# Kernel tuning notes

Measured on AMD Instinct MI355X. Metric: run time of the kernel, lower is better.

The kernel has to match this reference:

```python
import jax, jax.numpy as jnp
import numpy as np

N_NODES = 50000
N_EDGES = 640000
D = 128      # in_feats
OUT = 128    # out_feats


def setup_inputs() -> dict:
    key = jax.random.key(0)
    ks = jax.random.split(key, 8)
    feat = jax.random.normal(ks[0], (N_NODES, D), dtype=jnp.float32)
    weight = jax.random.uniform(ks[1], (N_EDGES,), dtype=jnp.float32)
    src = jax.random.randint(ks[2], (N_EDGES,), 0, N_NODES, dtype=jnp.int64)
    dst = jax.random.randint(ks[3], (N_EDGES,), 0, N_NODES, dtype=jnp.int64)
    # xavier_uniform with relu gain ~ sqrt(2)*sqrt(6/(fan_in+fan_out))
    g = np.sqrt(2.0)
    lim_pool = g * np.sqrt(6.0 / (D + D))
    lim_neigh = g * np.sqrt(6.0 / (2 * D + OUT))
    W_pool = jax.random.uniform(ks[4], (D, D), dtype=jnp.float32, minval=-lim_pool, maxval=lim_pool)
    b_pool = jnp.zeros((D,), dtype=jnp.float32)
    W_neigh = jax.random.uniform(ks[5], (OUT, 2 * D), dtype=jnp.float32, minval=-lim_neigh, maxval=lim_neigh)
    b_neigh = jnp.zeros((OUT,), dtype=jnp.float32)
    return {"feat": feat, "weight": weight, "src": src, "dst": dst,
            "W_pool": W_pool, "b_pool": b_pool, "W_neigh": W_neigh, "b_neigh": b_neigh}


def reference(feat, weight, src, dst, W_pool, b_pool, W_neigh, b_neigh):
    n = feat.shape[0]
    # fc_pool: h = feat @ W_pool.T + b_pool  -> [N, D]
    h = feat @ W_pool.T + b_pool
    # u_mul_e: per-edge message m_e = h[src_e] * w_e  -> [E, D]
    m = h[src] * weight[:, None]
    # max reduce over incoming edges (scatter-max by dst)
    neigh = jax.ops.segment_max(m, dst, num_segments=n)
    # zero-degree nodes get 0 (segment_max fills empties with -inf)
    deg = jax.ops.segment_sum(jnp.ones_like(weight), dst, num_segments=n)
    neigh = jnp.where(deg[:, None] > 0, neigh, jnp.zeros((), dtype=feat.dtype))
    # fc_neigh on concat(feat, neigh)
    rst = jnp.concatenate([feat, neigh], axis=1) @ W_neigh.T + b_neigh
    return rst
```

## Files before the change

### kernel.cpp

```cpp
#include <hip/hip_runtime.h>
#include <cstdint>
#include <cstddef>

#define N_NODES 50000
#define N_EDGES 640000
#define DF 128

#define NBUCK 196
#define BCAP  6144
#define ECAP  8192
#define PA_BLOCKS 250
#define DUMMY_ROW 50000

typedef __attribute__((ext_vector_type(8))) short bf16x8;
typedef __attribute__((ext_vector_type(4))) float f32x4;

__device__ inline unsigned short f2bf(float f) {
    unsigned int u = __float_as_uint(f);
    return (unsigned short)((u + 0x7fffu + ((u >> 16) & 1u)) >> 16);
}

#define NF4 (N_NODES * DF / 4)
#define NWG (3 * 2048)
__global__ __launch_bounds__(256) void k1_setup_bucket(
    const float* __restrict__ feat,
    const float* __restrict__ W_pool,
    const float* __restrict__ W_neigh,
    const int* __restrict__ src,
    const int* __restrict__ dst,
    const float* __restrict__ w,
    unsigned short* __restrict__ featb,
    unsigned short* __restrict__ hb,
    unsigned short* __restrict__ Wp_f,
    unsigned short* __restrict__ Wn1_f,
    unsigned short* __restrict__ Wn2_f,
    int* __restrict__ bucketcnt,
    uint2* __restrict__ staging)
{
    int bid = blockIdx.x;
    int t = threadIdx.x;
    if (bid < PA_BLOCKS) {
        __shared__ int cnt[NBUCK];
        __shared__ int runbase[NBUCK];
        int base = bid * 2560;
        if (t < NBUCK) cnt[t] = 0;
        __syncthreads();
        uint2 rec[10];
        int bk[10];
        #pragma unroll
        for (int i = 0; i < 10; ++i) {
            int e = base + i * 256 + t;
            int s = src[e], d = dst[e];
            bk[i] = d >> 8;
            rec[i].x = (unsigned int)s | ((unsigned int)(d & 255) << 16);
            rec[i].y = __float_as_uint(w[e]);
            atomicAdd(&cnt[bk[i]], 1);
        }
        __syncthreads();
        if (t < NBUCK) {
            runbase[t] = atomicAdd(&bucketcnt[t], cnt[t]);
            cnt[t] = 0;
        }
        __syncthreads();
        #pragma unroll
        for (int i = 0; i < 10; ++i) {
            int r = atomicAdd(&cnt[bk[i]], 1);
            int pos = runbase[bk[i]] + r;
            if (pos < BCAP) staging[bk[i] * BCAP + pos] = rec[i];
        }
    } else if (bid < 250 + NF4 / 256) {
        int idx = (bid - PA_BLOCKS) * 256 + t;
        float4 v = ((const float4*)feat)[idx];
        ushort4 o;
        o.x = f2bf(v.x); o.y = f2bf(v.y); o.z = f2bf(v.z); o.w = f2bf(v.w);
        ((ushort4*)featb)[idx] = o;
    } else if (bid < 250 + NF4 / 256 + NWG / 256) {
        int g = (bid - PA_BLOCKS - NF4 / 256) * 256 + t;
        int m = g >> 11;
        int r8 = g & 2047;
        int L = r8 & 63, tt = (r8 >> 6) & 3, c = r8 >> 8;
        int o = c * 16 + (L & 15);
        int kb = tt * 32 + (L >> 4) * 8;
        const float* srcp;
        unsigned short* dstp;
        if (m == 0)      { srcp = W_pool  + o * 128 + kb;       dstp = Wp_f;  }
        else if (m == 1) { srcp = W_neigh + o * 256 + kb;       dstp = Wn1_f; }
        else             { srcp = W_neigh + o * 256 + 128 + kb; dstp = Wn2_f; }
        ushort4 lo, hi;
        float4 a = ((const float4*)srcp)[0];
        float4 b = ((const float4*)srcp)[1];
        lo.x = f2bf(a.x); lo.y = f2bf(a.y); lo.z = f2bf(a.z); lo.w = f2bf(a.w);
        hi.x = f2bf(b.x); hi.y = f2bf(b.y); hi.z = f2bf(b.z); hi.w = f2bf(b.w);
        ((ushort4*)(dstp + r8 * 8))[0] = lo;
        ((ushort4*)(dstp + r8 * 8))[1] = hi;
    } else {
        if (t < DF) hb[(size_t)DUMMY_ROW * DF + t] = 0xFF7Fu;
    }
}

#define GEMMB 196
__global__ __launch_bounds__(1024) void k2_gemm_passb(
    const unsigned short* __restrict__ featb,
    const unsigned short* __restrict__ Wp_f,
    const float* __restrict__ b_pool,
    unsigned short* __restrict__ hb,
    const int* __restrict__ bucketcnt,
    const uint2* __restrict__ staging,
    int* __restrict__ offsets,
    int* __restrict__ nend,
    uint2* __restrict__ edges)
{
    int t = threadIdx.x;
    if (blockIdx.x < GEMMB) {
        int wave = blockIdx.x * 16 + (t >> 6);
        int lane = t & 63;
        int m0 = wave * 16;
        if (m0 >= N_NODES) return;
        const int n = lane & 15, quad = lane >> 4;

        f32x4 acc[8];
        #pragma unroll
        for (int c = 0; c < 8; ++c) {
            float bv = b_pool[c * 16 + n];
            acc[c] = (f32x4){bv, bv, bv, bv};
        }
        const unsigned short* aptr = featb + (size_t)(m0 + n) * DF + quad * 8;
        #pragma unroll
        for (int tt = 0; tt < 4; ++tt) {
            bf16x8 af = *(const bf16x8*)(aptr + tt * 32);
            #pragma unroll
            for (int c = 0; c < 8; ++c) {
                bf16x8 bf = *(const bf16x8*)(Wp_f + (size_t)((c * 4 + tt) * 64 + lane) * 8);
                acc[c] = __builtin_amdgcn_mfma_f32_16x16x32_bf16(af, bf, acc[c], 0, 0, 0);
            }
        }
        #pragma unroll
        for (int c = 0; c < 8; ++c)
            #pragma unroll
            for (int r = 0; r < 4; ++r)
                hb[(size_t)(m0 + quad * 4 + r) * DF + c * 16 + n] = f2bf(acc[c][r]);
    } else {
        __shared__ int dcnt[256];
        __shared__ int sc[256];
        int b = blockIdx.x - GEMMB;
        int cnt = bucketcnt[b];
        if (cnt > BCAP) cnt = BCAP;

        if (t < 256) dcnt[t] = 0;
        __syncthreads();

        uint2 rec[6];
        int nit = (cnt + 1023) >> 10;
        for (int i = 0; i < nit; ++i) {
            int idx = i * 1024 + t;
            if (idx < cnt) {
                rec[i] = staging[(size_t)b * BCAP + idx];
                atomicAdd(&dcnt[(rec[i].x >> 16) & 255], 1);
            }
        }
        __syncthreads();
        int mydeg = 0, mypad = 0;
        if (t < 256) {
            mydeg = dcnt[t];
            mypad = (mydeg + 7) & ~7;
            sc[t] = mypad;
        }
        __syncthreads();
        #pragma unroll
        for (int off = 1; off < 256; off <<= 1) {
            int u = (t < 256 && t >= off) ? sc[t - off] : 0;
            __syncthreads();
            if (t < 256) sc[t] += u;
            __syncthreads();
        }
        if (t < 256) {
            int beg = b * ECAP + sc[t] - mypad;
            int node = b * 256 + t;
            if (node < N_NODES) {
                offsets[node] = beg;
                nend[node] = beg + mypad;
            }
            dcnt[t] = beg;
            uint2 dmy; dmy.x = DUMMY_ROW; dmy.y = 0x3F800000u;
            for (int k = mydeg; k < mypad; ++k) edges[beg + k] = dmy;
        }
        __syncthreads();
        for (int i = 0; i < nit; ++i) {
            int idx = i * 1024 + t;
            if (idx < cnt) {
                int dl = (rec[i].x >> 16) & 255;
                int pos = atomicAdd(&dcnt[dl], 1);
                uint2 fin;
                fin.x = rec[i].x & 0xFFFFu;
                fin.y = rec[i].y;
                edges[pos] = fin;
            }
        }
    }
}

__global__ __launch_bounds__(256) void neigh_max_kernel(
    const unsigned short* __restrict__ hb, const int* __restrict__ offsets,
    const int* __restrict__ nend,
    const uint2* __restrict__ edges,
    unsigned short* __restrict__ neighb)
{
    int gwave = (blockIdx.x * 256 + threadIdx.x) >> 6;
    if (gwave >= N_NODES) return;
    int node = __builtin_amdgcn_readfirstlane(gwave);
    int lane = threadIdx.x & 63;
    const int half = lane >> 5;
    const int q = lane & 31;

    int beg = offsets[node], end = nend[node];
    float4 acc = make_float4(-3.4e38f, -3.4e38f, -3.4e38f, -3.4e38f);

    for (int e = beg; e < end; e += 8) {
        uint2 e0 = edges[e],     e1 = edges[e + 1], e2 = edges[e + 2], e3 = edges[e + 3];
        uint2 e4 = edges[e + 4], e5 = edges[e + 5], e6 = edges[e + 6], e7 = edges[e + 7];
        uint2 mA = half ? e1 : e0;
        uint2 mB = half ? e3 : e2;
        uint2 mC = half ? e5 : e4;
        uint2 mD = half ? e7 : e6;
        float wA = __uint_as_float(mA.y);
        float wB = __uint_as_float(mB.y);
        float wC = __uint_as_float(mC.y);
        float wD = __uint_as_float(mD.y);
        uint2 pA = *(const uint2*)(hb + (size_t)mA.x * DF + q * 4);
        uint2 pB = *(const uint2*)(hb + (size_t)mB.x * DF + q * 4);
        uint2 pC = *(const uint2*)(hb + (size_t)mC.x * DF + q * 4);
        uint2 pD = *(const uint2*)(hb + (size_t)mD.x * DF + q * 4);
        acc.x = fmaxf(acc.x, __uint_as_float(pA.x << 16)          * wA);
        acc.y = fmaxf(acc.y, __uint_as_float(pA.x & 0xffff0000u)  * wA);
        acc.z = fmaxf(acc.z, __uint_as_float(pA.y << 16)          * wA);
        acc.w = fmaxf(acc.w, __uint_as_float(pA.y & 0xffff0000u)  * wA);
        acc.x = fmaxf(acc.x, __uint_as_float(pB.x << 16)          * wB);
        acc.y = fmaxf(acc.y, __uint_as_float(pB.x & 0xffff0000u)  * wB);
        acc.z = fmaxf(acc.z, __uint_as_float(pB.y << 16)          * wB);
        acc.w = fmaxf(acc.w, __uint_as_float(pB.y & 0xffff0000u)  * wB);
        acc.x = fmaxf(acc.x, __uint_as_float(pC.x << 16)          * wC);
        acc.y = fmaxf(acc.y, __uint_as_float(pC.x & 0xffff0000u)  * wC);
        acc.z = fmaxf(acc.z, __uint_as_float(pC.y << 16)          * wC);
        acc.w = fmaxf(acc.w, __uint_as_float(pC.y & 0xffff0000u)  * wC);
        acc.x = fmaxf(acc.x, __uint_as_float(pD.x << 16)          * wD);
        acc.y = fmaxf(acc.y, __uint_as_float(pD.x & 0xffff0000u)  * wD);
        acc.z = fmaxf(acc.z, __uint_as_float(pD.y << 16)          * wD);
        acc.w = fmaxf(acc.w, __uint_as_float(pD.y & 0xffff0000u)  * wD);
    }

    float4 o;
    o.x = fmaxf(acc.x, __shfl_xor(acc.x, 32));
    o.y = fmaxf(acc.y, __shfl_xor(acc.y, 32));
    o.z = fmaxf(acc.z, __shfl_xor(acc.z, 32));
    o.w = fmaxf(acc.w, __shfl_xor(acc.w, 32));
    if (beg == end) o = make_float4(0.f, 0.f, 0.f, 0.f);
    if (half == 0) {
        ushort4 ob;
        ob.x = f2bf(o.x); ob.y = f2bf(o.y); ob.z = f2bf(o.z); ob.w = f2bf(o.w);
        *(ushort4*)(neighb + (size_t)node * DF + q * 4) = ob;
    }
}

__global__ __launch_bounds__(256) void gemm_out(
    const unsigned short* __restrict__ featb,
    const unsigned short* __restrict__ neighb,
    const unsigned short* __restrict__ Wn1_f,
    const unsigned short* __restrict__ Wn2_f,
    const float* __restrict__ bias,
    float* __restrict__ out)
{
    int wave = (blockIdx.x * 256 + threadIdx.x) >> 6;
    int lane = threadIdx.x & 63;
    int m0 = wave * 16;
    if (m0 >= N_NODES) return;
    const int n = lane & 15, quad = lane >> 4;

    f32x4 acc[8];
    #pragma unroll
    for (int c = 0; c < 8; ++c) {
        float bv = bias[c * 16 + n];
        acc[c] = (f32x4){bv, bv, bv, bv};
    }

    const unsigned short* a0 = featb  + (size_t)(m0 + n) * DF + quad * 8;
    const unsigned short* a1 = neighb + (size_t)(m0 + n) * DF + quad * 8;
    #pragma unroll
    for (int t = 0; t < 4; ++t) {
        bf16x8 af = *(const bf16x8*)(a0 + t * 32);
        #pragma unroll
        for (int c = 0; c < 8; ++c) {
            bf16x8 bf = *(const bf16x8*)(Wn1_f + (size_t)((c * 4 + t) * 64 + lane) * 8);
            acc[c] = __builtin_amdgcn_mfma_f32_16x16x32_bf16(af, bf, acc[c], 0, 0, 0);
        }
    }
    #pragma unroll
    for (int t = 0; t < 4; ++t) {
        bf16x8 af = *(const bf16x8*)(a1 + t * 32);
        #pragma unroll
        for (int c = 0; c < 8; ++c) {
            bf16x8 bf = *(const bf16x8*)(Wn2_f + (size_t)((c * 4 + t) * 64 + lane) * 8);
            acc[c] = __builtin_amdgcn_mfma_f32_16x16x32_bf16(af, bf, acc[c], 0, 0, 0);
        }
    }

    #pragma unroll
    for (int c = 0; c < 8; ++c)
        #pragma unroll
        for (int r = 0; r < 4; ++r)
            out[(size_t)(m0 + quad * 4 + r) * DF + c * 16 + n] = acc[c][r];
}

extern "C" void kernel_launch(void* const* d_in, const int* in_sizes, int n_in,
                              void* d_out, int out_size, void* d_ws, size_t ws_size,
                              hipStream_t stream) {
    const float* feat    = (const float*)d_in[0];
    const float* weight  = (const float*)d_in[1];
    const int*   src     = (const int*)d_in[2];
    const int*   dst     = (const int*)d_in[3];
    const float* W_pool  = (const float*)d_in[4];
    const float* b_pool  = (const float*)d_in[5];
    const float* W_neigh = (const float*)d_in[6];
    const float* b_neigh = (const float*)d_in[7];
    float* out = (float*)d_out;

    char* ws = (char*)d_ws;
    unsigned short* featb  = (unsigned short*)(ws);
    unsigned short* hb     = (unsigned short*)(ws + 12800000);
    unsigned short* Wp_f   = (unsigned short*)(ws + 25600512);
    unsigned short* Wn1_f  = (unsigned short*)(ws + 25633280);
    unsigned short* Wn2_f  = (unsigned short*)(ws + 25666048);
    int*   offsets   = (int*)  (ws + 25698816);
    int*   nend      = (int*)  (ws + 25898816);
    int*   bucketcnt = (int*)  (ws + 26098816);
    uint2* staging   = (uint2*)(ws + 26099840);
    uint2* edges     = (uint2*)(ws + 35733632);
    unsigned short* neighb = (unsigned short*)(ws + 48578688);

    hipMemsetAsync(bucketcnt, 0, 1024, stream);

    const int K1_BLOCKS = PA_BLOCKS + NF4 / 256 + NWG / 256 + 1;
    k1_setup_bucket<<<K1_BLOCKS, 256, 0, stream>>>(
        feat, W_pool, W_neigh, src, dst, weight,
        featb, hb, Wp_f, Wn1_f, Wn2_f, bucketcnt, staging);

    k2_gemm_passb<<<GEMMB + NBUCK, 1024, 0, stream>>>(
        featb, Wp_f, b_pool, hb, bucketcnt, staging, offsets, nend, edges);

    neigh_max_kernel<<<(N_NODES + 3) / 4, 256, 0, stream>>>(
        hb, offsets, nend, edges, neighb);

    gemm_out<<<782, 256, 0, stream>>>(
        featb, neighb, Wn1_f, Wn2_f, b_neigh, out);
}
```

Before: 162.3 us.

## Replace two-pass bucket sort with fixed-slot atomic scatter and fuse pool GEMM

```diff
diff --git a/kernel.cpp b/kernel.cpp
--- a/kernel.cpp
+++ b/kernel.cpp
@@ -5,12 +5,11 @@
 #define N_NODES 50000
 #define N_EDGES 640000
 #define DF 128
-
-#define NBUCK 196
-#define BCAP  6144
-#define ECAP  8192
-#define PA_BLOCKS 250
-#define DUMMY_ROW 50000
+#define SLOT 64
+
+#define SC_BLOCKS 625
+#define GEMM_BLOCKS 782
+#define FRAG_BLOCKS 16
 
 typedef __attribute__((ext_vector_type(8))) short bf16x8;
 typedef __attribute__((ext_vector_type(4))) float f32x4;
@@ -20,72 +19,98 @@
     return (unsigned short)((u + 0x7fffu + ((u >> 16) & 1u)) >> 16);
 }
 
-#define NF4 (N_NODES * DF / 4)
-#define NWG (3 * 2048)
-__global__ __launch_bounds__(256) void k1_setup_bucket(
+__global__ __launch_bounds__(256) void k1_scatter_gemm(
     const float* __restrict__ feat,
     const float* __restrict__ W_pool,
     const float* __restrict__ W_neigh,
+    const float* __restrict__ b_pool,
     const int* __restrict__ src,
     const int* __restrict__ dst,
     const float* __restrict__ w,
     unsigned short* __restrict__ featb,
     unsigned short* __restrict__ hb,
-    unsigned short* __restrict__ Wp_f,
     unsigned short* __restrict__ Wn1_f,
     unsigned short* __restrict__ Wn2_f,
-    int* __restrict__ bucketcnt,
-    uint2* __restrict__ staging)
+    int* __restrict__ cnt,
+    uint2* __restrict__ edges)
 {
     int bid = blockIdx.x;
     int t = threadIdx.x;
-    if (bid < PA_BLOCKS) {
-        __shared__ int cnt[NBUCK];
-        __shared__ int runbase[NBUCK];
-        int base = bid * 2560;
-        if (t < NBUCK) cnt[t] = 0;
+    if (bid < SC_BLOCKS) {
+        int base = bid * 1024;
+        #pragma unroll
+        for (int k = 0; k < 4; ++k) {
+            int e = base + k * 256 + t;
+            int s = src[e], d = dst[e];
+            float wv = w[e];
+            int c = atomicAdd(&cnt[d], 1);
+            if (c < SLOT) {
+                uint2 r; r.x = (unsigned int)s; r.y = __float_as_uint(wv);
+                edges[(size_t)d * SLOT + c] = r;
+            }
+        }
+    } else if (bid < SC_BLOCKS + GEMM_BLOCKS) {
+        __shared__ __align__(16) unsigned short wsh[16384];
+        #pragma unroll
+        for (int k = 0; k < 8; ++k) {
+            int r8 = t * 8 + k;
+            int L = r8 & 63, tt2 = (r8 >> 6) & 3, c = r8 >> 8;
+            const float* srcp = W_pool + (c * 16 + (L & 15)) * 128
+                                       + tt2 * 32 + (L >> 4) * 8;
+            float4 a = ((const float4*)srcp)[0];
+            float4 b = ((const float4*)srcp)[1];
+            ushort4 lo, hi;
+            lo.x = f2bf(a.x); lo.y = f2bf(a.y); lo.z = f2bf(a.z); lo.w = f2bf(a.w);
+            hi.x = f2bf(b.x); hi.y = f2bf(b.y); hi.z = f2bf(b.z); hi.w = f2bf(b.w);
+            ((ushort4*)(wsh + r8 * 8))[0] = lo;
+            ((ushort4*)(wsh + r8 * 8))[1] = hi;
+        }
         __syncthreads();
-        uint2 rec[10];
-        int bk[10];
-        #pragma unroll
-        for (int i = 0; i < 10; ++i) {
-            int e = base + i * 256 + t;
-            int s = src[e], d = dst[e];
-            bk[i] = d >> 8;
-            rec[i].x = (unsigned int)s | ((unsigned int)(d & 255) << 16);
-            rec[i].y = __float_as_uint(w[e]);
-            atomicAdd(&cnt[bk[i]], 1);
-        }
-        __syncthreads();
-        if (t < NBUCK) {
-            runbase[t] = atomicAdd(&bucketcnt[t], cnt[t]);
-            cnt[t] = 0;
-        }
-        __syncthreads();
-        #pragma unroll
-        for (int i = 0; i < 10; ++i) {
-            int r = atomicAdd(&cnt[bk[i]], 1);
-            int pos = runbase[bk[i]] + r;
-            if (pos < BCAP) staging[bk[i] * BCAP + pos] = rec[i];
-        }
-    } else if (bid < 250 + NF4 / 256) {
-        int idx = (bid - PA_BLOCKS) * 256 + t;
-        float4 v = ((const float4*)feat)[idx];
-        ushort4 o;
-        o.x = f2bf(v.x); o.y = f2bf(v.y); o.z = f2bf(v.z); o.w = f2bf(v.w);
-        ((ushort4*)featb)[idx] = o;
-    } else if (bid < 250 + NF4 / 256 + NWG / 256) {
-        int g = (bid - PA_BLOCKS - NF4 / 256) * 256 + t;
+
+        int gwave = (bid - SC_BLOCKS) * 4 + (t >> 6);
+        int m0 = gwave * 16;
+        if (m0 < N_NODES) {
+            int lane = t & 63;
+            const int n = lane & 15, quad = lane >> 4;
+            f32x4 acc[8];
+            #pragma unroll
+            for (int c = 0; c < 8; ++c) {
+                float bv = b_pool[c * 16 + n];
+                acc[c] = (f32x4){bv, bv, bv, bv};
+            }
+            const float* fp = feat + (size_t)(m0 + n) * DF + quad * 8;
+            unsigned short* fbp = featb + (size_t)(m0 + n) * DF + quad * 8;
+            #pragma unroll
+            for (int tt = 0; tt < 4; ++tt) {
+                float4 a = ((const float4*)(fp + tt * 32))[0];
+                float4 b = ((const float4*)(fp + tt * 32))[1];
+                union { bf16x8 v; ushort4 u4[2]; } af;
+                af.u4[0].x = f2bf(a.x); af.u4[0].y = f2bf(a.y);
+                af.u4[0].z = f2bf(a.z); af.u4[0].w = f2bf(a.w);
+                af.u4[1].x = f2bf(b.x); af.u4[1].y = f2bf(b.y);
+                af.u4[1].z = f2bf(b.z); af.u4[1].w = f2bf(b.w);
+                *(bf16x8*)(fbp + tt * 32) = af.v;
+                #pragma unroll
+                for (int c = 0; c < 8; ++c) {
+                    bf16x8 bfv = *(const bf16x8*)(wsh + (size_t)((c * 4 + tt) * 64 + lane) * 8);
+                    acc[c] = __builtin_amdgcn_mfma_f32_16x16x32_bf16(af.v, bfv, acc[c], 0, 0, 0);
+                }
+            }
+            #pragma unroll
+            for (int c = 0; c < 8; ++c)
+                #pragma unroll
+                for (int r = 0; r < 4; ++r)
+                    hb[(size_t)(m0 + quad * 4 + r) * DF + c * 16 + n] = f2bf(acc[c][r]);
+        }
+    } else {
+        int g = (bid - SC_BLOCKS - GEMM_BLOCKS) * 256 + t;
         int m = g >> 11;
         int r8 = g & 2047;
         int L = r8 & 63, tt = (r8 >> 6) & 3, c = r8 >> 8;
         int o = c * 16 + (L & 15);
         int kb = tt * 32 + (L >> 4) * 8;
-        const float* srcp;
-        unsigned short* dstp;
-        if (m == 0)      { srcp = W_pool  + o * 128 + kb;       dstp = Wp_f;  }
-        else if (m == 1) { srcp = W_neigh + o * 256 + kb;       dstp = Wn1_f; }
-        else             { srcp = W_neigh + o * 256 + 128 + kb; dstp = Wn2_f; }
+        const float* srcp = W_neigh + o * 256 + (m ? 128 : 0) + kb;
+        unsigned short* dstp = m ? Wn2_f : Wn1_f;
         ushort4 lo, hi;
         float4 a = ((const float4*)srcp)[0];
         float4 b = ((const float4*)srcp)[1];
@@ -93,115 +118,12 @@
         hi.x = f2bf(b.x); hi.y = f2bf(b.y); hi.z = f2bf(b.z); hi.w = f2bf(b.w);
         ((ushort4*)(dstp + r8 * 8))[0] = lo;
         ((ushort4*)(dstp + r8 * 8))[1] = hi;
-    } else {
-        if (t < DF) hb[(size_t)DUMMY_ROW * DF + t] = 0xFF7Fu;
-    }
-}
-
-#define GEMMB 196
-__global__ __launch_bounds__(1024) void k2_gemm_passb(
-    const unsigned short* __restrict__ featb,
-    const unsigned short* __restrict__ Wp_f,
-    const float* __restrict__ b_pool,
-    unsigned short* __restrict__ hb,
-    const int* __restrict__ bucketcnt,
-    const uint2* __restrict__ staging,
-    int* __restrict__ offsets,
-    int* __restrict__ nend,
-    uint2* __restrict__ edges)
-{
-    int t = threadIdx.x;
-    if (blockIdx.x < GEMMB) {
-        int wave = blockIdx.x * 16 + (t >> 6);
-        int lane = t & 63;
-        int m0 = wave * 16;
-        if (m0 >= N_NODES) return;
-        const int n = lane & 15, quad = lane >> 4;
-
-        f32x4 acc[8];
-        #pragma unroll
-        for (int c = 0; c < 8; ++c) {
-            float bv = b_pool[c * 16 + n];
-            acc[c] = (f32x4){bv, bv, bv, bv};
-        }
-        const unsigned short* aptr = featb + (size_t)(m0 + n) * DF + quad * 8;
-        #pragma unroll
-        for (int tt = 0; tt < 4; ++tt) {
-            bf16x8 af = *(const bf16x8*)(aptr + tt * 32);
-            #pragma unroll
-            for (int c = 0; c < 8; ++c) {
-                bf16x8 bf = *(const bf16x8*)(Wp_f + (size_t)((c * 4 + tt) * 64 + lane) * 8);
-                acc[c] = __builtin_amdgcn_mfma_f32_16x16x32_bf16(af, bf, acc[c], 0, 0, 0);
-            }
-        }
-        #pragma unroll
-        for (int c = 0; c < 8; ++c)
-            #pragma unroll
-            for (int r = 0; r < 4; ++r)
-                hb[(size_t)(m0 + quad * 4 + r) * DF + c * 16 + n] = f2bf(acc[c][r]);
-    } else {
-        __shared__ int dcnt[256];
-        __shared__ int sc[256];
-        int b = blockIdx.x - GEMMB;
-        int cnt = bucketcnt[b];
-        if (cnt > BCAP) cnt = BCAP;
-
-        if (t < 256) dcnt[t] = 0;
-        __syncthreads();
-
-        uint2 rec[6];
-        int nit = (cnt + 1023) >> 10;
-        for (int i = 0; i < nit; ++i) {
-            int idx = i * 1024 + t;
-            if (idx < cnt) {
-                rec[i] = staging[(size_t)b * BCAP + idx];
-                atomicAdd(&dcnt[(rec[i].x >> 16) & 255], 1);
-            }
-        }
-        __syncthreads();
-        int mydeg = 0, mypad = 0;
-        if (t < 256) {
-            mydeg = dcnt[t];
-            mypad = (mydeg + 7) & ~7;
-            sc[t] = mypad;
-        }
-        __syncthreads();
-        #pragma unroll
-        for (int off = 1; off < 256; off <<= 1) {
-            int u = (t < 256 && t >= off) ? sc[t - off] : 0;
-            __syncthreads();
-            if (t < 256) sc[t] += u;
-            __syncthreads();
-        }
-        if (t < 256) {
-            int beg = b * ECAP + sc[t] - mypad;
-            int node = b * 256 + t;
-            if (node < N_NODES) {
-                offsets[node] = beg;
-                nend[node] = beg + mypad;
-            }
-            dcnt[t] = beg;
-            uint2 dmy; dmy.x = DUMMY_ROW; dmy.y = 0x3F800000u;
-            for (int k = mydeg; k < mypad; ++k) edges[beg + k] = dmy;
-        }
-        __syncthreads();
-        for (int i = 0; i < nit; ++i) {
-            int idx = i * 1024 + t;
-            if (idx < cnt) {
-                int dl = (rec[i].x >> 16) & 255;
-                int pos = atomicAdd(&dcnt[dl], 1);
-                uint2 fin;
-                fin.x = rec[i].x & 0xFFFFu;
-                fin.y = rec[i].y;
-                edges[pos] = fin;
-            }
-        }
     }
 }
 
 __global__ __launch_bounds__(256) void neigh_max_kernel(
-    const unsigned short* __restrict__ hb, const int* __restrict__ offsets,
-    const int* __restrict__ nend,
+    const unsigned short* __restrict__ hb,
+    const int* __restrict__ cnt,
     const uint2* __restrict__ edges,
     unsigned short* __restrict__ neighb)
 {
@@ -212,12 +134,21 @@
     const int half = lane >> 5;
     const int q = lane & 31;
 
-    int beg = offsets[node], end = nend[node];
+    int beg = node * SLOT;
+    int dg = cnt[node]; if (dg > SLOT) dg = SLOT;
+    int end = beg + dg;
     float4 acc = make_float4(-3.4e38f, -3.4e38f, -3.4e38f, -3.4e38f);
 
     for (int e = beg; e < end; e += 8) {
-        uint2 e0 = edges[e],     e1 = edges[e + 1], e2 = edges[e + 2], e3 = edges[e + 3];
-        uint2 e4 = edges[e + 4], e5 = edges[e + 5], e6 = edges[e + 6], e7 = edges[e + 7];
+        int i1 = min(e + 1, end - 1);
+        int i2 = min(e + 2, end - 1);
+        int i3 = min(e + 3, end - 1);
+        int i4 = min(e + 4, end - 1);
+        int i5 = min(e + 5, end - 1);
+        int i6 = min(e + 6, end - 1);
+        int i7 = min(e + 7, end - 1);
+        uint2 e0 = edges[e],  e1 = edges[i1], e2 = edges[i2], e3 = edges[i3];
+        uint2 e4 = edges[i4], e5 = edges[i5], e6 = edges[i6], e7 = edges[i7];
         uint2 mA = half ? e1 : e0;
         uint2 mB = half ? e3 : e2;
         uint2 mC = half ? e5 : e4;
@@ -253,7 +184,7 @@
     o.y = fmaxf(acc.y, __shfl_xor(acc.y, 32));
     o.z = fmaxf(acc.z, __shfl_xor(acc.z, 32));
     o.w = fmaxf(acc.w, __shfl_xor(acc.w, 32));
-    if (beg == end) o = make_float4(0.f, 0.f, 0.f, 0.f);
+    if (dg == 0) o = make_float4(0.f, 0.f, 0.f, 0.f);
     if (half == 0) {
         ushort4 ob;
         ob.x = f2bf(o.x); ob.y = f2bf(o.y); ob.z = f2bf(o.z); ob.w = f2bf(o.w);
@@ -326,28 +257,21 @@
     char* ws = (char*)d_ws;
     unsigned short* featb  = (unsigned short*)(ws);
     unsigned short* hb     = (unsigned short*)(ws + 12800000);
-    unsigned short* Wp_f   = (unsigned short*)(ws + 25600512);
-    unsigned short* Wn1_f  = (unsigned short*)(ws + 25633280);
-    unsigned short* Wn2_f  = (unsigned short*)(ws + 25666048);
-    int*   offsets   = (int*)  (ws + 25698816);
-    int*   nend      = (int*)  (ws + 25898816);
-    int*   bucketcnt = (int*)  (ws + 26098816);
-    uint2* staging   = (uint2*)(ws + 26099840);
-    uint2* edges     = (uint2*)(ws + 35733632);
-    unsigned short* neighb = (unsigned short*)(ws + 48578688);
-
-    hipMemsetAsync(bucketcnt, 0, 1024, stream);
-
-    const int K1_BLOCKS = PA_BLOCKS + NF4 / 256 + NWG / 256 + 1;
-    k1_setup_bucket<<<K1_BLOCKS, 256, 0, stream>>>(
-        feat, W_pool, W_neigh, src, dst, weight,
-        featb, hb, Wp_f, Wn1_f, Wn2_f, bucketcnt, staging);
-
-    k2_gemm_passb<<<GEMMB + NBUCK, 1024, 0, stream>>>(
-        featb, Wp_f, b_pool, hb, bucketcnt, staging, offsets, nend, edges);
+    unsigned short* Wn1_f  = (unsigned short*)(ws + 25600000);
+    unsigned short* Wn2_f  = (unsigned short*)(ws + 25632768);
+    int*   cnt       = (int*)  (ws + 25665536);
+    uint2* edges     = (uint2*)(ws + 25865536);
+    unsigned short* neighb = (unsigned short*)(ws + 51465536);
+
+    hipMemsetAsync(cnt, 0, N_NODES * sizeof(int), stream);
+
+    const int K1_BLOCKS = SC_BLOCKS + GEMM_BLOCKS + FRAG_BLOCKS;
+    k1_scatter_gemm<<<K1_BLOCKS, 256, 0, stream>>>(
+        feat, W_pool, W_neigh, b_pool, src, dst, weight,
+        featb, hb, Wn1_f, Wn2_f, cnt, edges);
 
     neigh_max_kernel<<<(N_NODES + 3) / 4, 256, 0, stream>>>(
-        hb, offsets, nend, edges, neighb);
+        hb, cnt, edges, neighb);
 
     gemm_out<<<782, 256, 0, stream>>>(
         featb, neighb, Wn1_f, Wn2_f, b_neigh, out);
```

Measured after the change: 171.1 us. 1.05x slower.

## Fuse feat bf16 conversion into GEMMs and stage W_pool fragments in LDS

Applied to the files above, without the earlier changes.

```diff
diff --git a/kernel.cpp b/kernel.cpp
--- a/kernel.cpp
+++ b/kernel.cpp
@@ -10,6 +10,7 @@
 #define BCAP  6144
 #define ECAP  8192
 #define PA_BLOCKS 250
+#define FRAG_BLOCKS 16
 #define DUMMY_ROW 50000
 
 typedef __attribute__((ext_vector_type(8))) short bf16x8;
@@ -20,18 +21,12 @@
     return (unsigned short)((u + 0x7fffu + ((u >> 16) & 1u)) >> 16);
 }
 
-#define NF4 (N_NODES * DF / 4)
-#define NWG (3 * 2048)
-__global__ __launch_bounds__(256) void k1_setup_bucket(
-    const float* __restrict__ feat,
-    const float* __restrict__ W_pool,
+__global__ __launch_bounds__(256) void k1_passa_frags(
     const float* __restrict__ W_neigh,
     const int* __restrict__ src,
     const int* __restrict__ dst,
     const float* __restrict__ w,
-    unsigned short* __restrict__ featb,
     unsigned short* __restrict__ hb,
-    unsigned short* __restrict__ Wp_f,
     unsigned short* __restrict__ Wn1_f,
     unsigned short* __restrict__ Wn2_f,
     int* __restrict__ bucketcnt,
@@ -68,24 +63,15 @@
             int pos = runbase[bk[i]] + r;
             if (pos < BCAP) staging[bk[i] * BCAP + pos] = rec[i];
         }
-    } else if (bid < 250 + NF4 / 256) {
-        int idx = (bid - PA_BLOCKS) * 256 + t;
-        float4 v = ((const float4*)feat)[idx];
-        ushort4 o;
-        o.x = f2bf(v.x); o.y = f2bf(v.y); o.z = f2bf(v.z); o.w = f2bf(v.w);
-        ((ushort4*)featb)[idx] = o;
-    } else if (bid < 250 + NF4 / 256 + NWG / 256) {
-        int g = (bid - PA_BLOCKS - NF4 / 256) * 256 + t;
+    } else if (bid < PA_BLOCKS + FRAG_BLOCKS) {
+        int g = (bid - PA_BLOCKS) * 256 + t;
         int m = g >> 11;
         int r8 = g & 2047;
         int L = r8 & 63, tt = (r8 >> 6) & 3, c = r8 >> 8;
         int o = c * 16 + (L & 15);
         int kb = tt * 32 + (L >> 4) * 8;
-        const float* srcp;
-        unsigned short* dstp;
-        if (m == 0)      { srcp = W_pool  + o * 128 + kb;       dstp = Wp_f;  }
-        else if (m == 1) { srcp = W_neigh + o * 256 + kb;       dstp = Wn1_f; }
-        else             { srcp = W_neigh + o * 256 + 128 + kb; dstp = Wn2_f; }
+        const float* srcp = W_neigh + o * 256 + (m ? 128 : 0) + kb;
+        unsigned short* dstp = m ? Wn2_f : Wn1_f;
         ushort4 lo, hi;
         float4 a = ((const float4*)srcp)[0];
         float4 b = ((const float4*)srcp)[1];
@@ -100,8 +86,8 @@
 
 #define GEMMB 196
 __global__ __launch_bounds__(1024) void k2_gemm_passb(
-    const unsigned short* __restrict__ featb,
-    const unsigned short* __restrict__ Wp_f,
+    const float* __restrict__ feat,
+    const float* __restrict__ W_pool,
     const float* __restrict__ b_pool,
     unsigned short* __restrict__ hb,
     const int* __restrict__ bucketcnt,
@@ -112,26 +98,48 @@
 {
     int t = threadIdx.x;
     if (blockIdx.x < GEMMB) {
+        __shared__ __align__(16) unsigned short wsh[16384];
+        #pragma unroll
+        for (int k = 0; k < 2; ++k) {
+            int r8 = k * 1024 + t;
+            int L = r8 & 63, tt2 = (r8 >> 6) & 3, c = r8 >> 8;
+            const float* srcp = W_pool + (c * 16 + (L & 15)) * 128
+                                       + tt2 * 32 + (L >> 4) * 8;
+            float4 a = ((const float4*)srcp)[0];
+            float4 b = ((const float4*)srcp)[1];
+            ushort4 lo, hi;
+            lo.x = f2bf(a.x); lo.y = f2bf(a.y); lo.z = f2bf(a.z); lo.w = f2bf(a.w);
+            hi.x = f2bf(b.x); hi.y = f2bf(b.y); hi.z = f2bf(b.z); hi.w = f2bf(b.w);
+            ((ushort4*)(wsh + r8 * 8))[0] = lo;
+            ((ushort4*)(wsh + r8 * 8))[1] = hi;
+        }
+        __syncthreads();
+
         int wave = blockIdx.x * 16 + (t >> 6);
-        int lane = t & 63;
         int m0 = wave * 16;
         if (m0 >= N_NODES) return;
+        int lane = t & 63;
         const int n = lane & 15, quad = lane >> 4;
-
         f32x4 acc[8];
         #pragma unroll
         for (int c = 0; c < 8; ++c) {
             float bv = b_pool[c * 16 + n];
             acc[c] = (f32x4){bv, bv, bv, bv};
         }
-        const unsigned short* aptr = featb + (size_t)(m0 + n) * DF + quad * 8;
+        const float* fp = feat + (size_t)(m0 + n) * DF + quad * 8;
         #pragma unroll
         for (int tt = 0; tt < 4; ++tt) {
-            bf16x8 af = *(const bf16x8*)(aptr + tt * 32);
+            float4 a = ((const float4*)(fp + tt * 32))[0];
+            float4 b = ((const float4*)(fp + tt * 32))[1];
+            union { bf16x8 v; ushort4 u4[2]; } af;
+            af.u4[0].x = f2bf(a.x); af.u4[0].y = f2bf(a.y);
+            af.u4[0].z = f2bf(a.z); af.u4[0].w = f2bf(a.w);
+            af.u4[1].x = f2bf(b.x); af.u4[1].y = f2bf(b.y);
+            af.u4[1].z = f2bf(b.z); af.u4[1].w = f2bf(b.w);
             #pragma unroll
             for (int c = 0; c < 8; ++c) {
-                bf16x8 bf = *(const bf16x8*)(Wp_f + (size_t)((c * 4 + tt) * 64 + lane) * 8);
-                acc[c] = __builtin_amdgcn_mfma_f32_16x16x32_bf16(af, bf, acc[c], 0, 0, 0);
+                bf16x8 bfv = *(const bf16x8*)(wsh + (size_t)((c * 4 + tt) * 64 + lane) * 8);
+                acc[c] = __builtin_amdgcn_mfma_f32_16x16x32_bf16(af.v, bfv, acc[c], 0, 0, 0);
             }
         }
         #pragma unroll
@@ -262,7 +270,7 @@
 }
 
 __global__ __launch_bounds__(256) void gemm_out(
-    const unsigned short* __restrict__ featb,
+    const float* __restrict__ feat,
     const unsigned short* __restrict__ neighb,
     const unsigned short* __restrict__ Wn1_f,
     const unsigned short* __restrict__ Wn2_f,
@@ -282,15 +290,21 @@
         acc[c] = (f32x4){bv, bv, bv, bv};
     }
 
-    const unsigned short* a0 = featb  + (size_t)(m0 + n) * DF + quad * 8;
+    const float* a0 = feat + (size_t)(m0 + n) * DF + quad * 8;
     const unsigned short* a1 = neighb + (size_t)(m0 + n) * DF + quad * 8;
     #pragma unroll
     for (int t = 0; t < 4; ++t) {
-        bf16x8 af = *(const bf16x8*)(a0 + t * 32);
+        float4 a = ((const float4*)(a0 + t * 32))[0];
+        float4 b = ((const float4*)(a0 + t * 32))[1];
+        union { bf16x8 v; ushort4 u4[2]; } af;
+        af.u4[0].x = f2bf(a.x); af.u4[0].y = f2bf(a.y);
+        af.u4[0].z = f2bf(a.z); af.u4[0].w = f2bf(a.w);
+        af.u4[1].x = f2bf(b.x); af.u4[1].y = f2bf(b.y);
+        af.u4[1].z = f2bf(b.z); af.u4[1].w = f2bf(b.w);
         #pragma unroll
         for (int c = 0; c < 8; ++c) {
             bf16x8 bf = *(const bf16x8*)(Wn1_f + (size_t)((c * 4 + t) * 64 + lane) * 8);
-            acc[c] = __builtin_amdgcn_mfma_f32_16x16x32_bf16(af, bf, acc[c], 0, 0, 0);
+            acc[c] = __builtin_amdgcn_mfma_f32_16x16x32_bf16(af.v, bf, acc[c], 0, 0, 0);
         }
     }
     #pragma unroll
@@ -324,31 +338,28 @@
     float* out = (float*)d_out;
 
     char* ws = (char*)d_ws;
-    unsigned short* featb  = (unsigned short*)(ws);
-    unsigned short* hb     = (unsigned short*)(ws + 12800000);
-    unsigned short* Wp_f   = (unsigned short*)(ws + 25600512);
-    unsigned short* Wn1_f  = (unsigned short*)(ws + 25633280);
-    unsigned short* Wn2_f  = (unsigned short*)(ws + 25666048);
-    int*   offsets   = (int*)  (ws + 25698816);
-    int*   nend      = (int*)  (ws + 25898816);
-    int*   bucketcnt = (int*)  (ws + 26098816);
-    uint2* staging   = (uint2*)(ws + 26099840);
-    uint2* edges     = (uint2*)(ws + 35733632);
-    unsigned short* neighb = (unsigned short*)(ws + 48578688);
+    unsigned short* hb     = (unsigned short*)(ws);
+    unsigned short* Wn1_f  = (unsigned short*)(ws + 12800256);
+    unsigned short* Wn2_f  = (unsigned short*)(ws + 12833024);
+    int*   offsets   = (int*)  (ws + 12865792);
+    int*   nend      = (int*)  (ws + 13065792);
+    int*   bucketcnt = (int*)  (ws + 13265792);
+    uint2* staging   = (uint2*)(ws + 13266816);
+    uint2* edges     = (uint2*)(ws + 22900608);
+    unsigned short* neighb = (unsigned short*)(ws + 35745664);
 
     hipMemsetAsync(bucketcnt, 0, 1024, stream);
 
-    const int K1_BLOCKS = PA_BLOCKS + NF4 / 256 + NWG / 256 + 1;
-    k1_setup_bucket<<<K1_BLOCKS, 256, 0, stream>>>(
-        feat, W_pool, W_neigh, src, dst, weight,
-        featb, hb, Wp_f, Wn1_f, Wn2_f, bucketcnt, staging);
+    const int K1_BLOCKS = PA_BLOCKS + FRAG_BLOCKS + 1;
+    k1_passa_frags<<<K1_BLOCKS, 256, 0, stream>>>(
+        W_neigh, src, dst, weight, hb, Wn1_f, Wn2_f, bucketcnt, staging);
 
     k2_gemm_passb<<<GEMMB + NBUCK, 1024, 0, stream>>>(
-        featb, Wp_f, b_pool, hb, bucketcnt, staging, offsets, nend, edges);
+        feat, W_pool, b_pool, hb, bucketcnt, staging, offsets, nend, edges);
 
     neigh_max_kernel<<<(N_NODES + 3) / 4, 256, 0, stream>>>(
         hb, offsets, nend, edges, neighb);
 
     gemm_out<<<782, 256, 0, stream>>>(
-        featb, neighb, Wn1_f, Wn2_f, b_neigh, out);
-}
+        feat, neighb, Wn1_f, Wn2_f, b_neigh, out);
+}
```

Result: slower. 169.1 us (+4.2%).

## Replace CSR build and per-node gather with bucketed LDS atomic-max aggregation

Applied to the files above, without the earlier changes.

```diff
diff --git a/kernel.cpp b/kernel.cpp
--- a/kernel.cpp
+++ b/kernel.cpp
@@ -6,11 +6,9 @@
 #define N_EDGES 640000
 #define DF 128
 
-#define NBUCK 196
-#define BCAP  6144
-#define ECAP  8192
+#define NBUCK 782
+#define BCAP  1280
 #define PA_BLOCKS 250
-#define DUMMY_ROW 50000
 
 typedef __attribute__((ext_vector_type(8))) short bf16x8;
 typedef __attribute__((ext_vector_type(4))) float f32x4;
@@ -19,10 +17,17 @@
     unsigned int u = __float_as_uint(f);
     return (unsigned short)((u + 0x7fffu + ((u >> 16) & 1u)) >> 16);
 }
+__device__ inline unsigned int encf(float f) {
+    unsigned int u = __float_as_uint(f);
+    return (u & 0x80000000u) ? ~u : (u | 0x80000000u);
+}
+__device__ inline float decf(unsigned int e) {
+    return __uint_as_float((e & 0x80000000u) ? (e & 0x7FFFFFFFu) : ~e);
+}
 
 #define NF4 (N_NODES * DF / 4)
 #define NWG (3 * 2048)
-__global__ __launch_bounds__(256) void k1_setup_bucket(
+__global__ __launch_bounds__(256) void k1_passa_featb_frags(
     const float* __restrict__ feat,
     const float* __restrict__ W_pool,
     const float* __restrict__ W_neigh,
@@ -30,7 +35,6 @@
     const int* __restrict__ dst,
     const float* __restrict__ w,
     unsigned short* __restrict__ featb,
-    unsigned short* __restrict__ hb,
     unsigned short* __restrict__ Wp_f,
     unsigned short* __restrict__ Wn1_f,
     unsigned short* __restrict__ Wn2_f,
@@ -43,7 +47,7 @@
         __shared__ int cnt[NBUCK];
         __shared__ int runbase[NBUCK];
         int base = bid * 2560;
-        if (t < NBUCK) cnt[t] = 0;
+        for (int i = t; i < NBUCK; i += 256) cnt[i] = 0;
         __syncthreads();
         uint2 rec[10];
         int bk[10];
@@ -51,22 +55,22 @@
         for (int i = 0; i < 10; ++i) {
             int e = base + i * 256 + t;
             int s = src[e], d = dst[e];
-            bk[i] = d >> 8;
-            rec[i].x = (unsigned int)s | ((unsigned int)(d & 255) << 16);
+            bk[i] = d >> 6;
+            rec[i].x = (unsigned int)s | ((unsigned int)(d & 63) << 16);
             rec[i].y = __float_as_uint(w[e]);
             atomicAdd(&cnt[bk[i]], 1);
         }
         __syncthreads();
-        if (t < NBUCK) {
-            runbase[t] = atomicAdd(&bucketcnt[t], cnt[t]);
-            cnt[t] = 0;
+        for (int i = t; i < NBUCK; i += 256) {
+            runbase[i] = atomicAdd(&bucketcnt[i], cnt[i]);
+            cnt[i] = 0;
         }
         __syncthreads();
         #pragma unroll
         for (int i = 0; i < 10; ++i) {
             int r = atomicAdd(&cnt[bk[i]], 1);
             int pos = runbase[bk[i]] + r;
-            if (pos < BCAP) staging[bk[i] * BCAP + pos] = rec[i];
+            if (pos < BCAP) staging[(size_t)bk[i] * BCAP + pos] = rec[i];
         }
     } else if (bid < 250 + NF4 / 256) {
         int idx = (bid - PA_BLOCKS) * 256 + t;
@@ -74,7 +78,7 @@
         ushort4 o;
         o.x = f2bf(v.x); o.y = f2bf(v.y); o.z = f2bf(v.z); o.w = f2bf(v.w);
         ((ushort4*)featb)[idx] = o;
-    } else if (bid < 250 + NF4 / 256 + NWG / 256) {
+    } else {
         int g = (bid - PA_BLOCKS - NF4 / 256) * 256 + t;
         int m = g >> 11;
         int r8 = g & 2047;
@@ -93,171 +97,87 @@
         hi.x = f2bf(b.x); hi.y = f2bf(b.y); hi.z = f2bf(b.z); hi.w = f2bf(b.w);
         ((ushort4*)(dstp + r8 * 8))[0] = lo;
         ((ushort4*)(dstp + r8 * 8))[1] = hi;
-    } else {
-        if (t < DF) hb[(size_t)DUMMY_ROW * DF + t] = 0xFF7Fu;
-    }
-}
-
-#define GEMMB 196
-__global__ __launch_bounds__(1024) void k2_gemm_passb(
+    }
+}
+
+__global__ __launch_bounds__(256) void gemm_pool_kernel(
     const unsigned short* __restrict__ featb,
     const unsigned short* __restrict__ Wp_f,
     const float* __restrict__ b_pool,
-    unsigned short* __restrict__ hb,
+    unsigned short* __restrict__ hb)
+{
+    int wave = (blockIdx.x * 256 + threadIdx.x) >> 6;
+    int lane = threadIdx.x & 63;
+    int m0 = wave * 16;
+    if (m0 >= N_NODES) return;
+    const int n = lane & 15, quad = lane >> 4;
+
+    f32x4 acc[8];
+    #pragma unroll
+    for (int c = 0; c < 8; ++c) {
+        float bv = b_pool[c * 16 + n];
+        acc[c] = (f32x4){bv, bv, bv, bv};
+    }
+    const unsigned short* aptr = featb + (size_t)(m0 + n) * DF + quad * 8;
+    #pragma unroll
+    for (int tt = 0; tt < 4; ++tt) {
+        bf16x8 af = *(const bf16x8*)(aptr + tt * 32);
+        #pragma unroll
+        for (int c = 0; c < 8; ++c) {
+            bf16x8 bf = *(const bf16x8*)(Wp_f + (size_t)((c * 4 + tt) * 64 + lane) * 8);
+            acc[c] = __builtin_amdgcn_mfma_f32_16x16x32_bf16(af, bf, acc[c], 0, 0, 0);
+        }
+    }
+    #pragma unroll
+    for (int c = 0; c < 8; ++c)
+        #pragma unroll
+        for (int r = 0; r < 4; ++r)
+            hb[(size_t)(m0 + quad * 4 + r) * DF + c * 16 + n] = f2bf(acc[c][r]);
+}
+
+__global__ __launch_bounds__(512, 8) void bucket_max_kernel(
+    const unsigned short* __restrict__ hb,
     const int* __restrict__ bucketcnt,
     const uint2* __restrict__ staging,
-    int* __restrict__ offsets,
-    int* __restrict__ nend,
-    uint2* __restrict__ edges)
-{
-    int t = threadIdx.x;
-    if (blockIdx.x < GEMMB) {
-        int wave = blockIdx.x * 16 + (t >> 6);
-        int lane = t & 63;
-        int m0 = wave * 16;
-        if (m0 >= N_NODES) return;
-        const int n = lane & 15, quad = lane >> 4;
-
-        f32x4 acc[8];
-        #pragma unroll
-        for (int c = 0; c < 8; ++c) {
-            float bv = b_pool[c * 16 + n];
-            acc[c] = (f32x4){bv, bv, bv, bv};
-        }
-        const unsigned short* aptr = featb + (size_t)(m0 + n) * DF + quad * 8;
-        #pragma unroll
-        for (int tt = 0; tt < 4; ++tt) {
-            bf16x8 af = *(const bf16x8*)(aptr + tt * 32);
-            #pragma unroll
-            for (int c = 0; c < 8; ++c) {
-                bf16x8 bf = *(const bf16x8*)(Wp_f + (size_t)((c * 4 + tt) * 64 + lane) * 8);
-                acc[c] = __builtin_amdgcn_mfma_f32_16x16x32_bf16(af, bf, acc[c], 0, 0, 0);
-            }
-        }
-        #pragma unroll
-        for (int c = 0; c < 8; ++c)
-            #pragma unroll
-            for (int r = 0; r < 4; ++r)
-                hb[(size_t)(m0 + quad * 4 + r) * DF + c * 16 + n] = f2bf(acc[c][r]);
-    } else {
-        __shared__ int dcnt[256];
-        __shared__ int sc[256];
-        int b = blockIdx.x - GEMMB;
-        int cnt = bucketcnt[b];
-        if (cnt > BCAP) cnt = BCAP;
-
-        if (t < 256) dcnt[t] = 0;
-        __syncthreads();
-
-        uint2 rec[6];
-        int nit = (cnt + 1023) >> 10;
-        for (int i = 0; i < nit; ++i) {
-            int idx = i * 1024 + t;
-            if (idx < cnt) {
-                rec[i] = staging[(size_t)b * BCAP + idx];
-                atomicAdd(&dcnt[(rec[i].x >> 16) & 255], 1);
-            }
-        }
-        __syncthreads();
-        int mydeg = 0, mypad = 0;
-        if (t < 256) {
-            mydeg = dcnt[t];
-            mypad = (mydeg + 7) & ~7;
-            sc[t] = mypad;
-        }
-        __syncthreads();
-        #pragma unroll
-        for (int off = 1; off < 256; off <<= 1) {
-            int u = (t < 256 && t >= off) ? sc[t - off] : 0;
-            __syncthreads();
-            if (t < 256) sc[t] += u;
-            __syncthreads();
-        }
-        if (t < 256) {
-            int beg = b * ECAP + sc[t] - mypad;
-            int node = b * 256 + t;
-            if (node < N_NODES) {
-                offsets[node] = beg;
-                nend[node] = beg + mypad;
-            }
-            dcnt[t] = beg;
-            uint2 dmy; dmy.x = DUMMY_ROW; dmy.y = 0x3F800000u;
-            for (int k = mydeg; k < mypad; ++k) edges[beg + k] = dmy;
-        }
-        __syncthreads();
-        for (int i = 0; i < nit; ++i) {
-            int idx = i * 1024 + t;
-            if (idx < cnt) {
-                int dl = (rec[i].x >> 16) & 255;
-                int pos = atomicAdd(&dcnt[dl], 1);
-                uint2 fin;
-                fin.x = rec[i].x & 0xFFFFu;
-                fin.y = rec[i].y;
-                edges[pos] = fin;
-            }
-        }
-    }
-}
-
-__global__ __launch_bounds__(256) void neigh_max_kernel(
-    const unsigned short* __restrict__ hb, const int* __restrict__ offsets,
-    const int* __restrict__ nend,
-    const uint2* __restrict__ edges,
     unsigned short* __restrict__ neighb)
 {
-    int gwave = (blockIdx.x * 256 + threadIdx.x) >> 6;
-    if (gwave >= N_NODES) return;
-    int node = __builtin_amdgcn_readfirstlane(gwave);
-    int lane = threadIdx.x & 63;
-    const int half = lane >> 5;
-    const int q = lane & 31;
-
-    int beg = offsets[node], end = nend[node];
-    float4 acc = make_float4(-3.4e38f, -3.4e38f, -3.4e38f, -3.4e38f);
-
-    for (int e = beg; e < end; e += 8) {
-        uint2 e0 = edges[e],     e1 = edges[e + 1], e2 = edges[e + 2], e3 = edges[e + 3];
-        uint2 e4 = edges[e + 4], e5 = edges[e + 5], e6 = edges[e + 6], e7 = edges[e + 7];
-        uint2 mA = half ? e1 : e0;
-        uint2 mB = half ? e3 : e2;
-        uint2 mC = half ? e5 : e4;
-        uint2 mD = half ? e7 : e6;
-        float wA = __uint_as_float(mA.y);
-        float wB = __uint_as_float(mB.y);
-        float wC = __uint_as_float(mC.y);
-        float wD = __uint_as_float(mD.y);
-        uint2 pA = *(const uint2*)(hb + (size_t)mA.x * DF + q * 4);
-        uint2 pB = *(const uint2*)(hb + (size_t)mB.x * DF + q * 4);
-        uint2 pC = *(const uint2*)(hb + (size_t)mC.x * DF + q * 4);
-        uint2 pD = *(const uint2*)(hb + (size_t)mD.x * DF + q * 4);
-        acc.x = fmaxf(acc.x, __uint_as_float(pA.x << 16)          * wA);
-        acc.y = fmaxf(acc.y, __uint_as_float(pA.x & 0xffff0000u)  * wA);
-        acc.z = fmaxf(acc.z, __uint_as_float(pA.y << 16)          * wA);
-        acc.w = fmaxf(acc.w, __uint_as_float(pA.y & 0xffff0000u)  * wA);
-        acc.x = fmaxf(acc.x, __uint_as_float(pB.x << 16)          * wB);
-        acc.y = fmaxf(acc.y, __uint_as_float(pB.x & 0xffff0000u)  * wB);
-        acc.z = fmaxf(acc.z, __uint_as_float(pB.y << 16)          * wB);
-        acc.w = fmaxf(acc.w, __uint_as_float(pB.y & 0xffff0000u)  * wB);
-        acc.x = fmaxf(acc.x, __uint_as_float(pC.x << 16)          * wC);
-        acc.y = fmaxf(acc.y, __uint_as_float(pC.x & 0xffff0000u)  * wC);
-        acc.z = fmaxf(acc.z, __uint_as_float(pC.y << 16)          * wC);
-        acc.w = fmaxf(acc.w, __uint_as_float(pC.y & 0xffff0000u)  * wC);
-        acc.x = fmaxf(acc.x, __uint_as_float(pD.x << 16)          * wD);
-        acc.y = fmaxf(acc.y, __uint_as_float(pD.x & 0xffff0000u)  * wD);
-        acc.z = fmaxf(acc.z, __uint_as_float(pD.y << 16)          * wD);
-        acc.w = fmaxf(acc.w, __uint_as_float(pD.y & 0xffff0000u)  * wD);
-    }
-
-    float4 o;
-    o.x = fmaxf(acc.x, __shfl_xor(acc.x, 32));
-    o.y = fmaxf(acc.y, __shfl_xor(acc.y, 32));
-    o.z = fmaxf(acc.z, __shfl_xor(acc.z, 32));
-    o.w = fmaxf(acc.w, __shfl_xor(acc.w, 32));
-    if (beg == end) o = make_float4(0.f, 0.f, 0.f, 0.f);
-    if (half == 0) {
-        ushort4 ob;
-        ob.x = f2bf(o.x); ob.y = f2bf(o.y); ob.z = f2bf(o.z); ob.w = f2bf(o.w);
-        *(ushort4*)(neighb + (size_t)node * DF + q * 4) = ob;
+    __shared__ unsigned int mx[64 * DF];
+    __shared__ int deg[64];
+    const int t = threadIdx.x;
+    const int b = blockIdx.x;
+    int cnt = bucketcnt[b]; if (cnt > BCAP) cnt = BCAP;
+
+    for (int i = t; i < 64 * DF; i += 512) mx[i] = 0u;
+    if (t < 64) deg[t] = 0;
+    __syncthreads();
+
+    const int wid = t >> 6, lane = t & 63;
+    for (int i = wid; i < cnt; i += 8) {
+        uint2 rec = staging[(size_t)b * BCAP + i];
+        int dl = (rec.x >> 16) & 63;
+        int s  = rec.x & 0xFFFF;
+        float wv = __uint_as_float(rec.y);
+        unsigned int p = *(const unsigned int*)(hb + (size_t)s * DF + lane * 2);
+        float v0 = __uint_as_float(p << 16)          * wv;
+        float v1 = __uint_as_float(p & 0xffff0000u)  * wv;
+        atomicMax(&mx[dl * DF + lane * 2],     encf(v0));
+        atomicMax(&mx[dl * DF + lane * 2 + 1], encf(v1));
+        if (lane == 0) atomicAdd(&deg[dl], 1);
+    }
+    __syncthreads();
+
+    for (int j = t; j < 64 * 32; j += 512) {
+        int r = j >> 5, c4 = (j & 31) * 4;
+        int node = b * 64 + r;
+        if (node < N_NODES) {
+            bool nz = deg[r] > 0;
+            ushort4 ob;
+            ob.x = nz ? f2bf(decf(mx[r * DF + c4]))     : (unsigned short)0;
+            ob.y = nz ? f2bf(decf(mx[r * DF + c4 + 1])) : (unsigned short)0;
+            ob.z = nz ? f2bf(decf(mx[r * DF + c4 + 2])) : (unsigned short)0;
+            ob.w = nz ? f2bf(decf(mx[r * DF + c4 + 3])) : (unsigned short)0;
+            *(ushort4*)(neighb + (size_t)node * DF + c4) = ob;
+        }
     }
 }
 
@@ -326,28 +246,23 @@
     char* ws = (char*)d_ws;
     unsigned short* featb  = (unsigned short*)(ws);
     unsigned short* hb     = (unsigned short*)(ws + 12800000);
-    unsigned short* Wp_f   = (unsigned short*)(ws + 25600512);
-    unsigned short* Wn1_f  = (unsigned short*)(ws + 25633280);
-    unsigned short* Wn2_f  = (unsigned short*)(ws + 25666048);
-    int*   offsets   = (int*)  (ws + 25698816);
-    int*   nend      = (int*)  (ws + 25898816);
-    int*   bucketcnt = (int*)  (ws + 26098816);
-    uint2* staging   = (uint2*)(ws + 26099840);
-    uint2* edges     = (uint2*)(ws + 35733632);
-    unsigned short* neighb = (unsigned short*)(ws + 48578688);
-
-    hipMemsetAsync(bucketcnt, 0, 1024, stream);
-
-    const int K1_BLOCKS = PA_BLOCKS + NF4 / 256 + NWG / 256 + 1;
-    k1_setup_bucket<<<K1_BLOCKS, 256, 0, stream>>>(
+    unsigned short* Wp_f   = (unsigned short*)(ws + 25600000);
+    unsigned short* Wn1_f  = (unsigned short*)(ws + 25632768);
+    unsigned short* Wn2_f  = (unsigned short*)(ws + 25665536);
+    int*   bucketcnt = (int*)  (ws + 25698304);
+    uint2* staging   = (uint2*)(ws + 25701504);
+    unsigned short* neighb = (unsigned short*)(ws + 33709184);
+
+    hipMemsetAsync(bucketcnt, 0, NBUCK * sizeof(int), stream);
+
+    const int K1_BLOCKS = PA_BLOCKS + NF4 / 256 + NWG / 256;
+    k1_passa_featb_frags<<<K1_BLOCKS, 256, 0, stream>>>(
         feat, W_pool, W_neigh, src, dst, weight,
-        featb, hb, Wp_f, Wn1_f, Wn2_f, bucketcnt, staging);
-
-    k2_gemm_passb<<<GEMMB + NBUCK, 1024, 0, stream>>>(
-        featb, Wp_f, b_pool, hb, bucketcnt, staging, offsets, nend, edges);
-
-    neigh_max_kernel<<<(N_NODES + 3) / 4, 256, 0, stream>>>(
-        hb, offsets, nend, edges, neighb);
+        featb, Wp_f, Wn1_f, Wn2_f, bucketcnt, staging);
+
+    gemm_pool_kernel<<<782, 256, 0, stream>>>(featb, Wp_f, b_pool, hb);
+
+    bucket_max_kernel<<<NBUCK, 512, 0, stream>>>(hb, bucketcnt, staging, neighb);
 
     gemm_out<<<782, 256, 0, stream>>>(
         featb, neighb, Wn1_f, Wn2_f, b_neigh, out);
```

New measurement: 206.8 us. 27.4% more time.
